# Kernel optimization log

Hardware: AMD Instinct MI355X
Metric: run time of the kernel (lower is better)

The kernel has to match this reference:

```python
import jax, jax.numpy as jnp
import numpy as np

N_NODES = 100_000
N_EDGES = 1_600_000
D_IN, D_HID = 128, 256


def setup_inputs() -> dict:
    key = jax.random.key(0)
    k1, k2, k3, k4, k5 = jax.random.split(key, 5)
    x = jax.random.normal(k1, (N_NODES, D_IN), dtype=jnp.float32)
    edge_index = jax.random.randint(k2, (2, N_EDGES), 0, N_NODES, dtype=jnp.int64)
    # PyG Linear weights are [out_features, in_features]; glorot-ish scale
    W1 = jax.random.normal(k3, (D_HID, D_IN), dtype=jnp.float32) * (1.0 / np.sqrt(D_IN))
    W2 = jax.random.normal(k4, (D_HID, D_HID), dtype=jnp.float32) * (1.0 / np.sqrt(D_HID))
    W3 = jax.random.normal(k5, (D_HID, D_HID), dtype=jnp.float32) * (1.0 / np.sqrt(D_HID))
    return {"x": x, "edge_index": edge_index, "W1": W1, "W2": W2, "W3": W3}


def reference(x, edge_index, W1, W2, W3):
    N = x.shape[0]
    loop = jnp.arange(N, dtype=edge_index.dtype)
    # GCNConv default: add self-loops, symmetric normalization D^-1/2 (A+I) D^-1/2
    row = jnp.concatenate([edge_index[0], loop])  # source nodes
    col = jnp.concatenate([edge_index[1], loop])  # target nodes (aggregation)
    deg = jax.ops.segment_sum(jnp.ones(row.shape[0], dtype=x.dtype), col, num_segments=N)
    dinv = jnp.where(deg > 0, deg ** -0.5, 0.0)
    norm = dinv[row] * dinv[col]  # [E+N]

    def gcn_conv(h, W):
        h = h @ W.T                              # dense transform [N, out]
        msg = h[row] * norm[:, None]             # gather + scale   [E+N, out]
        return jax.ops.segment_sum(msg, col, num_segments=N)  # scatter-add

    h = jax.nn.relu(gcn_conv(x, W1))
    h = jax.nn.relu(gcn_conv(h, W2))
    return gcn_conv(h, W3)
```

## Files before the change

### kernel.cpp

```cpp
#include <hip/hip_runtime.h>


constexpr int DIN = 128;
constexpr int DH  = 256;

typedef _Float16 f16x8 __attribute__((ext_vector_type(8)));
typedef float    f32x4 __attribute__((ext_vector_type(4)));

__device__ __forceinline__ float h2f(unsigned short u) {
    _Float16 h;
    __builtin_memcpy(&h, &u, 2);
    return (float)h;
}
__device__ __forceinline__ unsigned short f2h(float f) {
    _Float16 h = (_Float16)f;
    unsigned short u;
    __builtin_memcpy(&u, &h, 2);
    return u;
}

__global__ void zero_int_kernel(int* __restrict__ p, int n) {
    int i = blockIdx.x * blockDim.x + threadIdx.x;
    if (i < n) p[i] = 0;
}

__global__ void count_deg_kernel(const int* __restrict__ col, int E, int* __restrict__ deg) {
    int e = blockIdx.x * blockDim.x + threadIdx.x;
    if (e < E) atomicAdd(&deg[col[e]], 1);
}

__global__ __launch_bounds__(256) void scan_p1_kernel(const int* __restrict__ deg,
                                                      int* __restrict__ bsum, int N) {
    int t = threadIdx.x;
    int base = blockIdx.x * 1024 + t * 4;
    int s = 0;
    #pragma unroll
    for (int k = 0; k < 4; k++) { int i = base + k; if (i < N) s += deg[i]; }
    __shared__ int red[256];
    red[t] = s;
    __syncthreads();
    for (int off = 128; off > 0; off >>= 1) {
        if (t < off) red[t] += red[t + off];
        __syncthreads();
    }
    if (t == 0) bsum[blockIdx.x] = red[0];
}

__global__ __launch_bounds__(1024) void scan_p2_kernel(int* __restrict__ bsum, int nb) {
    __shared__ int sums[1024];
    int t = threadIdx.x;
    int chunk = (nb + 1023) / 1024;
    int s0 = t * chunk, s1 = min(nb, s0 + chunk);
    int local = 0;
    for (int i = s0; i < s1; i++) local += bsum[i];
    sums[t] = local;
    __syncthreads();
    for (int off = 1; off < 1024; off <<= 1) {
        int v = (t >= off) ? sums[t - off] : 0;
        __syncthreads();
        sums[t] += v;
        __syncthreads();
    }
    int prefix = (t == 0) ? 0 : sums[t - 1];
    for (int i = s0; i < s1; i++) { int v = bsum[i]; bsum[i] = prefix; prefix += v; }
}

__global__ __launch_bounds__(256) void scan_p3_kernel(int* __restrict__ deg,
                                                      const int* __restrict__ bsum,
                                                      int* __restrict__ rowptr,
                                                      float* __restrict__ dinv,
                                                      int N, int E) {
    int t = threadIdx.x;
    int base = blockIdx.x * 1024 + t * 4;
    int v[4];
    int s = 0;
    #pragma unroll
    for (int k = 0; k < 4; k++) {
        int i = base + k;
        v[k] = (i < N) ? deg[i] : 0;
        s += v[k];
    }
    __shared__ int sums[256];
    sums[t] = s;
    __syncthreads();
    for (int off = 1; off < 256; off <<= 1) {
        int u = (t >= off) ? sums[t - off] : 0;
        __syncthreads();
        sums[t] += u;
        __syncthreads();
    }
    int prefix = bsum[blockIdx.x] + ((t == 0) ? 0 : sums[t - 1]);
    #pragma unroll
    for (int k = 0; k < 4; k++) {
        int i = base + k;
        if (i < N) {
            rowptr[i] = prefix;
            dinv[i] = 1.0f / sqrtf((float)(v[k] + 1));
            deg[i] = 0;
        }
        prefix += v[k];
    }
    if (blockIdx.x == 0 && t == 0) rowptr[N] = E;
}

__global__ void fill_csr_kernel(const int* __restrict__ row, const int* __restrict__ col,
                                const int* __restrict__ rowptr, int* __restrict__ cnt,
                                const float* __restrict__ dinv,
                                int* __restrict__ csr_src, float* __restrict__ csr_w, int E) {
    int e = blockIdx.x * blockDim.x + threadIdx.x;
    if (e >= E) return;
    int r = row[e], c = col[e];
    int pos = rowptr[c] + atomicAdd(&cnt[c], 1);
    csr_src[pos] = r;
    csr_w[pos]   = dinv[r] * dinv[c];
}

__global__ void cast_f16_kernel(const float4* __restrict__ in, ushort4* __restrict__ out, int n4) {
    int i = blockIdx.x * blockDim.x + threadIdx.x;
    if (i >= n4) return;
    float4 v = in[i];
    ushort4 o;
    o.x = f2h(v.x); o.y = f2h(v.y); o.z = f2h(v.z); o.w = f2h(v.w);
    out[i] = o;
}

template<int D>
__global__ __launch_bounds__(256) void agg_gather_f16_kernel(const int* __restrict__ rowptr,
                                                             const int* __restrict__ csr_src,
                                                             const float* __restrict__ csr_w,
                                                             const float* __restrict__ dinv,
                                                             const ushort4* __restrict__ in,
                                                             ushort4* __restrict__ out, int N) {
    constexpr int L = D / 4;
    constexpr int GPB = 256 / L;
    int n = blockIdx.x * GPB + threadIdx.x / L;
    if (n >= N) return;
    int lane = threadIdx.x % L;

    float di = dinv[n];
    float s = di * di;
    ushort4 sv = in[(size_t)n * L + lane];
    float4 acc = make_float4(h2f(sv.x) * s, h2f(sv.y) * s, h2f(sv.z) * s, h2f(sv.w) * s);

    int start = rowptr[n], end = rowptr[n + 1];
    for (int j0 = start; j0 < end; j0 += L) {
        int nb = end - j0; if (nb > L) nb = L;
        int   src = 0;
        float w   = 0.0f;
        if (lane < nb) { src = csr_src[j0 + lane]; w = csr_w[j0 + lane]; }

        int t = 0;
        for (; t + 8 <= nb; t += 8) {
            int   rr[8];
            float wv[8];
            #pragma unroll
            for (int u = 0; u < 8; ++u) {
                if constexpr (L == 64) {
                    rr[u] = __builtin_amdgcn_readlane(src, t + u);
                    wv[u] = __int_as_float(__builtin_amdgcn_readlane(__float_as_int(w), t + u));
                } else {
                    rr[u] = __shfl(src, t + u, L);
                    wv[u] = __shfl(w,   t + u, L);
                }
            }
            ushort4 vv[8];
            #pragma unroll
            for (int u = 0; u < 8; ++u) vv[u] = in[(size_t)rr[u] * L + lane];
            #pragma unroll
            for (int u = 0; u < 8; ++u) {
                acc.x += wv[u] * h2f(vv[u].x);
                acc.y += wv[u] * h2f(vv[u].y);
                acc.z += wv[u] * h2f(vv[u].z);
                acc.w += wv[u] * h2f(vv[u].w);
            }
        }
        for (; t < nb; ++t) {
            int   r;
            float ww;
            if constexpr (L == 64) {
                r  = __builtin_amdgcn_readlane(src, t);
                ww = __int_as_float(__builtin_amdgcn_readlane(__float_as_int(w), t));
            } else {
                r  = __shfl(src, t, L);
                ww = __shfl(w,   t, L);
            }
            ushort4 v = in[(size_t)r * L + lane];
            acc.x += ww * h2f(v.x); acc.y += ww * h2f(v.y);
            acc.z += ww * h2f(v.z); acc.w += ww * h2f(v.w);
        }
    }
    ushort4 o;
    o.x = f2h(acc.x); o.y = f2h(acc.y); o.z = f2h(acc.z); o.w = f2h(acc.w);
    out[(size_t)n * L + lane] = o;
}

template<int K, bool RELU, typename OT>
__global__ __launch_bounds__(256) void gemm_nt_mfma_kernel(const unsigned short* __restrict__ A,
                                                           const unsigned short* __restrict__ Wh,
                                                           OT* __restrict__ C, int N) {
    __shared__ __align__(16) unsigned short As[128 * 64];
    __shared__ __align__(16) unsigned short Ws[128 * 64];
    int tid  = threadIdx.x;
    int lane = tid & 63;
    int wave = tid >> 6;
    int wr = wave >> 1, wc = wave & 1;
    int m0 = blockIdx.x * 128;
    int c0 = blockIdx.y * 128;

    f32x4 acc[4][4];
    #pragma unroll
    for (int i = 0; i < 4; i++)
        #pragma unroll
        for (int j = 0; j < 4; j++)
            #pragma unroll
            for (int r = 0; r < 4; r++) acc[i][j][r] = 0.0f;

    int srow  = tid >> 3;
    int sslot = tid & 7;

    for (int k0 = 0; k0 < K; k0 += 64) {
        #pragma unroll
        for (int q = 0; q < 4; ++q) {
            int row = q * 32 + srow;
            int byteoff = row * 128 + ((sslot ^ (row & 7)) << 4);
            int gr = m0 + row;
            if (gr >= N) gr = N - 1;
            f16x8 va = *(const f16x8*)(A + (size_t)gr * K + k0 + sslot * 8);
            *(f16x8*)((char*)As + byteoff) = va;
            int gw = c0 + row;
            f16x8 vw = *(const f16x8*)(Wh + (size_t)gw * K + k0 + sslot * 8);
            *(f16x8*)((char*)Ws + byteoff) = vw;
        }
        __syncthreads();

        #pragma unroll
        for (int kk = 0; kk < 2; ++kk) {
            int slot = kk * 4 + (lane >> 4);
            f16x8 a[4], b[4];
            #pragma unroll
            for (int i = 0; i < 4; i++) {
                int row = wr * 64 + i * 16 + (lane & 15);
                a[i] = *(const f16x8*)((const char*)As + row * 128 + ((slot ^ (row & 7)) << 4));
            }
            #pragma unroll
            for (int j = 0; j < 4; j++) {
                int row = wc * 64 + j * 16 + (lane & 15);
                b[j] = *(const f16x8*)((const char*)Ws + row * 128 + ((slot ^ (row & 7)) << 4));
            }
            #pragma unroll
            for (int i = 0; i < 4; i++)
                #pragma unroll
                for (int j = 0; j < 4; j++)
                    acc[i][j] = __builtin_amdgcn_mfma_f32_16x16x32_f16(a[i], b[j], acc[i][j], 0, 0, 0);
        }
        __syncthreads();
    }

    int r4 = (lane >> 4) * 4;
    int cn = lane & 15;
    #pragma unroll
    for (int i = 0; i < 4; i++) {
        #pragma unroll
        for (int r = 0; r < 4; r++) {
            int g_r = m0 + wr * 64 + i * 16 + r4 + r;
            if (g_r >= N) continue;
            #pragma unroll
            for (int j = 0; j < 4; j++) {
                float v = acc[i][j][r];
                if (RELU) v = fmaxf(v, 0.f);
                int col = c0 + wc * 64 + j * 16 + cn;
                if constexpr (sizeof(OT) == 4) {
                    ((float*)C)[(size_t)g_r * DH + col] = v;
                } else {
                    ((unsigned short*)C)[(size_t)g_r * DH + col] = f2h(v);
                }
            }
        }
    }
}

extern "C" void kernel_launch(void* const* d_in, const int* in_sizes, int n_in,
                              void* d_out, int out_size, void* d_ws, size_t ws_size,
                              hipStream_t stream) {
    const float* x  = (const float*)d_in[0];
    const int*   ei = (const int*)d_in[1];
    const float* W1 = (const float*)d_in[2];
    const float* W2 = (const float*)d_in[3];
    const float* W3 = (const float*)d_in[4];
    float* out = (float*)d_out;

    int N = in_sizes[0] / DIN;
    int E = in_sizes[1] / 2;
    const int* row = ei;
    const int* col = ei + E;

    char* ws = (char*)d_ws;
    int*   deg     = (int*)ws;
    float* dinv    = (float*)(ws + 400000);
    int*   rowptr  = (int*)(ws + 800000);
    int*   csr_src = (int*)(ws + 1200016);
    float* csr_w   = (float*)(ws + 7600016);
    unsigned short* bufA = (unsigned short*)(ws + 14000128);
    unsigned short* w1h  = (unsigned short*)(ws + 65200128);
    unsigned short* w2h  = (unsigned short*)(ws + 65265664);
    unsigned short* w3h  = (unsigned short*)(ws + 65396736);
    int*   bsum    = (int*)(ws + 65527808);

    unsigned short* hb = (unsigned short*)d_out;

    dim3 b256(256);
    int nb = (N + 1023) / 1024;

    zero_int_kernel<<<dim3((N + 255) / 256), b256, 0, stream>>>(deg, N);
    count_deg_kernel<<<dim3((E + 255) / 256), b256, 0, stream>>>(col, E, deg);
    scan_p1_kernel<<<dim3(nb), b256, 0, stream>>>(deg, bsum, N);
    scan_p2_kernel<<<dim3(1), dim3(1024), 0, stream>>>(bsum, nb);
    scan_p3_kernel<<<dim3(nb), b256, 0, stream>>>(deg, bsum, rowptr, dinv, N, E);
    fill_csr_kernel<<<dim3((E + 255) / 256), b256, 0, stream>>>(
        row, col, rowptr, deg, dinv, csr_src, csr_w, E);

    cast_f16_kernel<<<dim3((N * (DIN / 4) + 255) / 256), b256, 0, stream>>>(
        (const float4*)x, (ushort4*)hb, N * (DIN / 4));
    cast_f16_kernel<<<dim3((DH * DIN / 4 + 255) / 256), b256, 0, stream>>>(
        (const float4*)W1, (ushort4*)w1h, DH * DIN / 4);
    cast_f16_kernel<<<dim3((DH * DH / 4 + 255) / 256), b256, 0, stream>>>(
        (const float4*)W2, (ushort4*)w2h, DH * DH / 4);
    cast_f16_kernel<<<dim3((DH * DH / 4 + 255) / 256), b256, 0, stream>>>(
        (const float4*)W3, (ushort4*)w3h, DH * DH / 4);

    dim3 ggrid((N + 127) / 128, 2);

    agg_gather_f16_kernel<DIN><<<dim3((N + 7) / 8), b256, 0, stream>>>(
        rowptr, csr_src, csr_w, dinv, (const ushort4*)hb, (ushort4*)bufA, N);
    gemm_nt_mfma_kernel<DIN, true, unsigned short><<<ggrid, b256, 0, stream>>>(
        bufA, w1h, hb, N);

    agg_gather_f16_kernel<DH><<<dim3((N + 3) / 4), b256, 0, stream>>>(
        rowptr, csr_src, csr_w, dinv, (const ushort4*)hb, (ushort4*)bufA, N);
    gemm_nt_mfma_kernel<DH, true, unsigned short><<<ggrid, b256, 0, stream>>>(
        bufA, w2h, hb, N);

    agg_gather_f16_kernel<DH><<<dim3((N + 3) / 4), b256, 0, stream>>>(
        rowptr, csr_src, csr_w, dinv, (const ushort4*)hb, (ushort4*)bufA, N);
    gemm_nt_mfma_kernel<DH, false, float><<<ggrid, b256, 0, stream>>>(
        bufA, w3h, out, N);
}
```

Baseline: 708.9 us.

## Factor symmetric normalization into node scaling and drop per-edge weights

Splits the D^-1/2 (A+I) D^-1/2 normalization into per-node scaling. Features are pre-scaled by dinv (in the input cast and in the GEMM epilogue), the aggregation becomes a plain sum, and the result is scaled by dinv[n] at the end. This removes the csr_w array and its per-edge loads and multiplies. CSR fill now reuses the atomic slot recorded during degree counting instead of a second atomic pass. The GEMM grid is also remapped to 1D so both column tiles of a row block run adjacently for better L2 reuse. Rounding to fp16 at pre-scaled values changes numerics slightly.

```diff
diff --git a/kernel.cpp b/kernel.cpp
--- a/kernel.cpp
+++ b/kernel.cpp
@@ -24,9 +24,10 @@
     if (i < n) p[i] = 0;
 }
 
-__global__ void count_deg_kernel(const int* __restrict__ col, int E, int* __restrict__ deg) {
+__global__ void count_deg_kernel(const int* __restrict__ col, int E,
+                                 int* __restrict__ deg, int* __restrict__ seq) {
     int e = blockIdx.x * blockDim.x + threadIdx.x;
-    if (e < E) atomicAdd(&deg[col[e]], 1);
+    if (e < E) seq[e] = atomicAdd(&deg[col[e]], 1);
 }
 
 __global__ __launch_bounds__(256) void scan_p1_kernel(const int* __restrict__ deg,
@@ -65,7 +66,7 @@
     for (int i = s0; i < s1; i++) { int v = bsum[i]; bsum[i] = prefix; prefix += v; }
 }
 
-__global__ __launch_bounds__(256) void scan_p3_kernel(int* __restrict__ deg,
+__global__ __launch_bounds__(256) void scan_p3_kernel(const int* __restrict__ deg,
                                                       const int* __restrict__ bsum,
                                                       int* __restrict__ rowptr,
                                                       float* __restrict__ dinv,
@@ -96,7 +97,6 @@
         if (i < N) {
             rowptr[i] = prefix;
             dinv[i] = 1.0f / sqrtf((float)(v[k] + 1));
-            deg[i] = 0;
         }
         prefix += v[k];
     }
@@ -104,15 +104,12 @@
 }
 
 __global__ void fill_csr_kernel(const int* __restrict__ row, const int* __restrict__ col,
-                                const int* __restrict__ rowptr, int* __restrict__ cnt,
-                                const float* __restrict__ dinv,
-                                int* __restrict__ csr_src, float* __restrict__ csr_w, int E) {
+                                const int* __restrict__ seq, const int* __restrict__ rowptr,
+                                int* __restrict__ csr_src, int E) {
     int e = blockIdx.x * blockDim.x + threadIdx.x;
     if (e >= E) return;
-    int r = row[e], c = col[e];
-    int pos = rowptr[c] + atomicAdd(&cnt[c], 1);
-    csr_src[pos] = r;
-    csr_w[pos]   = dinv[r] * dinv[c];
+    int c = col[e];
+    csr_src[rowptr[c] + seq[e]] = row[e];
 }
 
 __global__ void cast_f16_kernel(const float4* __restrict__ in, ushort4* __restrict__ out, int n4) {
@@ -124,10 +121,21 @@
     out[i] = o;
 }
 
+__global__ void cast_f16_scaled_kernel(const float4* __restrict__ in,
+                                       const float* __restrict__ dinv,
+                                       ushort4* __restrict__ out, int n4) {
+    int i = blockIdx.x * blockDim.x + threadIdx.x;
+    if (i >= n4) return;
+    float s = dinv[i >> 5];
+    float4 v = in[i];
+    ushort4 o;
+    o.x = f2h(v.x * s); o.y = f2h(v.y * s); o.z = f2h(v.z * s); o.w = f2h(v.w * s);
+    out[i] = o;
+}
+
 template<int D>
 __global__ __launch_bounds__(256) void agg_gather_f16_kernel(const int* __restrict__ rowptr,
                                                              const int* __restrict__ csr_src,
-                                                             const float* __restrict__ csr_w,
                                                              const float* __restrict__ dinv,
                                                              const ushort4* __restrict__ in,
                                                              ushort4* __restrict__ out, int N) {
@@ -137,75 +145,68 @@
     if (n >= N) return;
     int lane = threadIdx.x % L;
 
-    float di = dinv[n];
-    float s = di * di;
     ushort4 sv = in[(size_t)n * L + lane];
-    float4 acc = make_float4(h2f(sv.x) * s, h2f(sv.y) * s, h2f(sv.z) * s, h2f(sv.w) * s);
+    float4 acc = make_float4(h2f(sv.x), h2f(sv.y), h2f(sv.z), h2f(sv.w));
 
     int start = rowptr[n], end = rowptr[n + 1];
     for (int j0 = start; j0 < end; j0 += L) {
         int nb = end - j0; if (nb > L) nb = L;
-        int   src = 0;
-        float w   = 0.0f;
-        if (lane < nb) { src = csr_src[j0 + lane]; w = csr_w[j0 + lane]; }
+        int src = (lane < nb) ? csr_src[j0 + lane] : 0;
 
         int t = 0;
         for (; t + 8 <= nb; t += 8) {
-            int   rr[8];
-            float wv[8];
+            int rr[8];
             #pragma unroll
             for (int u = 0; u < 8; ++u) {
-                if constexpr (L == 64) {
-                    rr[u] = __builtin_amdgcn_readlane(src, t + u);
-                    wv[u] = __int_as_float(__builtin_amdgcn_readlane(__float_as_int(w), t + u));
-                } else {
-                    rr[u] = __shfl(src, t + u, L);
-                    wv[u] = __shfl(w,   t + u, L);
-                }
+                if constexpr (L == 64) rr[u] = __builtin_amdgcn_readlane(src, t + u);
+                else                   rr[u] = __shfl(src, t + u, L);
             }
             ushort4 vv[8];
             #pragma unroll
             for (int u = 0; u < 8; ++u) vv[u] = in[(size_t)rr[u] * L + lane];
             #pragma unroll
             for (int u = 0; u < 8; ++u) {
-                acc.x += wv[u] * h2f(vv[u].x);
-                acc.y += wv[u] * h2f(vv[u].y);
-                acc.z += wv[u] * h2f(vv[u].z);
-                acc.w += wv[u] * h2f(vv[u].w);
+                acc.x += h2f(vv[u].x);
+                acc.y += h2f(vv[u].y);
+                acc.z += h2f(vv[u].z);
+                acc.w += h2f(vv[u].w);
             }
         }
         for (; t < nb; ++t) {
-            int   r;
-            float ww;
-            if constexpr (L == 64) {
-                r  = __builtin_amdgcn_readlane(src, t);
-                ww = __int_as_float(__builtin_amdgcn_readlane(__float_as_int(w), t));
-            } else {
-                r  = __shfl(src, t, L);
-                ww = __shfl(w,   t, L);
-            }
+            int r;
+            if constexpr (L == 64) r = __builtin_amdgcn_readlane(src, t);
+            else                   r = __shfl(src, t, L);
             ushort4 v = in[(size_t)r * L + lane];
-            acc.x += ww * h2f(v.x); acc.y += ww * h2f(v.y);
-            acc.z += ww * h2f(v.z); acc.w += ww * h2f(v.w);
-        }
-    }
+            acc.x += h2f(v.x); acc.y += h2f(v.y);
+            acc.z += h2f(v.z); acc.w += h2f(v.w);
+        }
+    }
+    float s = dinv[n];
     ushort4 o;
-    o.x = f2h(acc.x); o.y = f2h(acc.y); o.z = f2h(acc.z); o.w = f2h(acc.w);
+    o.x = f2h(acc.x * s); o.y = f2h(acc.y * s); o.z = f2h(acc.z * s); o.w = f2h(acc.w * s);
     out[(size_t)n * L + lane] = o;
 }
 
-template<int K, bool RELU, typename OT>
+template<int K, bool RELU, bool SCALE, typename OT>
 __global__ __launch_bounds__(256) void gemm_nt_mfma_kernel(const unsigned short* __restrict__ A,
                                                            const unsigned short* __restrict__ Wh,
-                                                           OT* __restrict__ C, int N) {
+                                                           OT* __restrict__ C,
+                                                           const float* __restrict__ dinv, int N) {
     __shared__ __align__(16) unsigned short As[128 * 64];
     __shared__ __align__(16) unsigned short Ws[128 * 64];
     int tid  = threadIdx.x;
     int lane = tid & 63;
     int wave = tid >> 6;
     int wr = wave >> 1, wc = wave & 1;
-    int m0 = blockIdx.x * 128;
-    int c0 = blockIdx.y * 128;
+
+    int nwgx = (N + 127) / 128;
+    int T = (2 * nwgx) & ~15;
+    int b = blockIdx.x;
+    int cx, cy;
+    if (b < T) { cx = (b >> 4) * 8 + (b & 7); cy = (b >> 3) & 1; }
+    else       { int rem = b - T; cx = (T >> 1) + (rem >> 1); cy = rem & 1; }
+    int m0 = cx * 128;
+    int c0 = cy * 128;
 
     f32x4 acc[4][4];
     #pragma unroll
@@ -236,7 +237,7 @@
         #pragma unroll
         for (int kk = 0; kk < 2; ++kk) {
             int slot = kk * 4 + (lane >> 4);
-            f16x8 a[4], b[4];
+            f16x8 a[4], bfr[4];
             #pragma unroll
             for (int i = 0; i < 4; i++) {
                 int row = wr * 64 + i * 16 + (lane & 15);
@@ -245,13 +246,13 @@
             #pragma unroll
             for (int j = 0; j < 4; j++) {
                 int row = wc * 64 + j * 16 + (lane & 15);
-                b[j] = *(const f16x8*)((const char*)Ws + row * 128 + ((slot ^ (row & 7)) << 4));
+                bfr[j] = *(const f16x8*)((const char*)Ws + row * 128 + ((slot ^ (row & 7)) << 4));
             }
             #pragma unroll
             for (int i = 0; i < 4; i++)
                 #pragma unroll
                 for (int j = 0; j < 4; j++)
-                    acc[i][j] = __builtin_amdgcn_mfma_f32_16x16x32_f16(a[i], b[j], acc[i][j], 0, 0, 0);
+                    acc[i][j] = __builtin_amdgcn_mfma_f32_16x16x32_f16(a[i], bfr[j], acc[i][j], 0, 0, 0);
         }
         __syncthreads();
     }
@@ -264,10 +265,12 @@
         for (int r = 0; r < 4; r++) {
             int g_r = m0 + wr * 64 + i * 16 + r4 + r;
             if (g_r >= N) continue;
+            float dv = SCALE ? dinv[g_r] : 1.0f;
             #pragma unroll
             for (int j = 0; j < 4; j++) {
                 float v = acc[i][j][r];
                 if (RELU) v = fmaxf(v, 0.f);
+                if (SCALE) v *= dv;
                 int col = c0 + wc * 64 + j * 16 + cn;
                 if constexpr (sizeof(OT) == 4) {
                     ((float*)C)[(size_t)g_r * DH + col] = v;
@@ -299,7 +302,7 @@
     float* dinv    = (float*)(ws + 400000);
     int*   rowptr  = (int*)(ws + 800000);
     int*   csr_src = (int*)(ws + 1200016);
-    float* csr_w   = (float*)(ws + 7600016);
+    int*   seq     = (int*)(ws + 7600016);
     unsigned short* bufA = (unsigned short*)(ws + 14000128);
     unsigned short* w1h  = (unsigned short*)(ws + 65200128);
     unsigned short* w2h  = (unsigned short*)(ws + 65265664);
@@ -312,15 +315,15 @@
     int nb = (N + 1023) / 1024;
 
     zero_int_kernel<<<dim3((N + 255) / 256), b256, 0, stream>>>(deg, N);
-    count_deg_kernel<<<dim3((E + 255) / 256), b256, 0, stream>>>(col, E, deg);
+    count_deg_kernel<<<dim3((E + 255) / 256), b256, 0, stream>>>(col, E, deg, seq);
     scan_p1_kernel<<<dim3(nb), b256, 0, stream>>>(deg, bsum, N);
     scan_p2_kernel<<<dim3(1), dim3(1024), 0, stream>>>(bsum, nb);
     scan_p3_kernel<<<dim3(nb), b256, 0, stream>>>(deg, bsum, rowptr, dinv, N, E);
     fill_csr_kernel<<<dim3((E + 255) / 256), b256, 0, stream>>>(
-        row, col, rowptr, deg, dinv, csr_src, csr_w, E);
-
-    cast_f16_kernel<<<dim3((N * (DIN / 4) + 255) / 256), b256, 0, stream>>>(
-        (const float4*)x, (ushort4*)hb, N * (DIN / 4));
+        row, col, seq, rowptr, csr_src, E);
+
+    cast_f16_scaled_kernel<<<dim3((N * (DIN / 4) + 255) / 256), b256, 0, stream>>>(
+        (const float4*)x, dinv, (ushort4*)hb, N * (DIN / 4));
     cast_f16_kernel<<<dim3((DH * DIN / 4 + 255) / 256), b256, 0, stream>>>(
         (const float4*)W1, (ushort4*)w1h, DH * DIN / 4);
     cast_f16_kernel<<<dim3((DH * DH / 4 + 255) / 256), b256, 0, stream>>>(
@@ -328,20 +331,20 @@
     cast_f16_kernel<<<dim3((DH * DH / 4 + 255) / 256), b256, 0, stream>>>(
         (const float4*)W3, (ushort4*)w3h, DH * DH / 4);
 
-    dim3 ggrid((N + 127) / 128, 2);
+    int nwg = 2 * ((N + 127) / 128);
 
     agg_gather_f16_kernel<DIN><<<dim3((N + 7) / 8), b256, 0, stream>>>(
-        rowptr, csr_src, csr_w, dinv, (const ushort4*)hb, (ushort4*)bufA, N);
-    gemm_nt_mfma_kernel<DIN, true, unsigned short><<<ggrid, b256, 0, stream>>>(
-        bufA, w1h, hb, N);
+        rowptr, csr_src, dinv, (const ushort4*)hb, (ushort4*)bufA, N);
+    gemm_nt_mfma_kernel<DIN, true, true, unsigned short><<<dim3(nwg), b256, 0, stream>>>(
+        bufA, w1h, hb, dinv, N);
 
     agg_gather_f16_kernel<DH><<<dim3((N + 3) / 4), b256, 0, stream>>>(
-        rowptr, csr_src, csr_w, dinv, (const ushort4*)hb, (ushort4*)bufA, N);
-    gemm_nt_mfma_kernel<DH, true, unsigned short><<<ggrid, b256, 0, stream>>>(
-        bufA, w2h, hb, N);
+        rowptr, csr_src, dinv, (const ushort4*)hb, (ushort4*)bufA, N);
+    gemm_nt_mfma_kernel<DH, true, true, unsigned short><<<dim3(nwg), b256, 0, stream>>>(
+        bufA, w2h, hb, dinv, N);
 
     agg_gather_f16_kernel<DH><<<dim3((N + 3) / 4), b256, 0, stream>>>(
-        rowptr, csr_src, csr_w, dinv, (const ushort4*)hb, (ushort4*)bufA, N);
-    gemm_nt_mfma_kernel<DH, false, float><<<ggrid, b256, 0, stream>>>(
-        bufA, w3h, out, N);
-}
+        rowptr, csr_src, dinv, (const ushort4*)hb, (ushort4*)bufA, N);
+    gemm_nt_mfma_kernel<DH, false, false, float><<<dim3(nwg), b256, 0, stream>>>(
+        bufA, w3h, out, dinv, N);
+}
```

Result: faster. 644.2 us (-9.1%).
